# Kernel tuning notes

Measured on AMD Instinct MI355X. Metric: run time of the kernel, lower is better.

## Reference

```python
import jax, jax.numpy as jnp
import numpy as np


def setup_inputs() -> dict:
    key = jax.random.key(0)
    k1, k2, k3 = jax.random.split(key, 3)
    B, S, IN, OUT = 4, 2048, 4096, 4096
    # int8 activations, weights, bias (stored as int8; math accumulates in int32)
    x = jax.random.randint(k1, (B, S, IN), -127, 128, dtype=jnp.int32).astype(jnp.int8)
    weight = jax.random.randint(k2, (OUT, IN), -127, 128, dtype=jnp.int32).astype(jnp.int8)  # (out, in)
    bias = jax.random.randint(k3, (1, OUT), -127, 128, dtype=jnp.int32).astype(jnp.int8)
    alpha = jnp.float32(0.001)  # input_scale*weight_scale/output_scale
    beta = jnp.float32(0.01)    # bias_scale/output_scale
    return {"x": x, "weight": weight, "bias": bias, "alpha": alpha, "beta": beta}


def reference(x, weight, bias, alpha, beta):
    # Flatten leading dims: (B,S,IN) -> (N,IN)
    x_shape = x.shape
    xf = x.reshape(-1, x_shape[-1])
    acc = jax.lax.dot_general(
        xf, weight,
        dimension_numbers=(((1,), (1,)), ((), ())),
        preferred_element_type=jnp.int32,
    )  # (N, OUT) int32
    # Fused epilogue: y = round(alpha*acc + beta*bias), saturate to int8
    yf = alpha * acc.astype(jnp.float32) + beta * bias.astype(jnp.float32)
    y = jnp.clip(jnp.round(yf), -128.0, 127.0).astype(jnp.int8)
    return y.reshape(*x_shape[:-1], -1)
```

## Files before the change

kernel.cpp:

```cpp
#include <hip/hip_runtime.h>
#include <stdint.h>

using i32x4  = __attribute__((ext_vector_type(4)))  int;
using i32x16 = __attribute__((ext_vector_type(16))) int;

#define M_TOT 8192
#define N_TOT 4096
#define K_TOT 4096
#define BM 256
#define BN 256
#define BK 128
#define NT (K_TOT / BK)

__device__ __forceinline__ void gload_lds16(const void* g, void* l) {
  __builtin_amdgcn_global_load_lds(
      (const __attribute__((address_space(1))) void*)(uintptr_t)g,
      (__attribute__((address_space(3))) void*)(uint32_t)(uintptr_t)l,
      16, 0, 0);
}

__global__ void pack_tiles(const int* __restrict__ in, int8_t* __restrict__ out, int ngroups) {
  int stride = gridDim.x * blockDim.x;
  for (int idx = blockIdx.x * blockDim.x + threadIdx.x; idx < ngroups; idx += stride) {
    int sp = idx & 3;
    int rr = (idx >> 2) & 255;
    int kc = (idx >> 10) & 63;
    int p  = idx >> 16;
    int sl = sp ^ ((rr >> 1) & 3);
    const i32x4* src = (const i32x4*)(in + (((size_t)(p * 256 + rr)) << 12) + kc * 64 + sl * 16);
    i32x4 a = src[0], b = src[1], c = src[2], d = src[3];
    i32x4 o;
    o.x = (a.x & 255) | ((a.y & 255) << 8) | ((a.z & 255) << 16) | (a.w << 24);
    o.y = (b.x & 255) | ((b.y & 255) << 8) | ((b.z & 255) << 16) | (b.w << 24);
    o.z = (c.x & 255) | ((c.y & 255) << 8) | ((c.z & 255) << 16) | (c.w << 24);
    o.w = (d.x & 255) | ((d.y & 255) << 8) | ((d.z & 255) << 16) | (d.w << 24);
    ((i32x4*)out)[idx] = o;
  }
}

#define STAGE(srcbase, kc, ldsbuf, isB, h)                                          \
  { const int8_t* _g = (srcbase) + (size_t)(kc) * 16384 + w * 2048 + l * 16;        \
    char* _d = &lds[ldsbuf][(isB) * 32768 + (h) * 16384 + w * 2048];                \
    gload_lds16(_g, _d);                                                            \
    gload_lds16(_g + 1024, _d + 1024); }

__global__ __launch_bounds__(512, 2) void gemm_w8a8(
    const int8_t* __restrict__ Apack,
    const int8_t* __restrict__ Bpack,
    const int*    __restrict__ bias,
    const float*  __restrict__ alphap,
    const float*  __restrict__ betap,
    int* __restrict__ out)
{
  __shared__ __align__(16) char lds[2][65536];

  const int bid = blockIdx.x;
  const int wg  = (bid & 7) * 64 + (bid >> 3);
  const int tm  = wg & 31;
  const int tn  = wg >> 5;

  const int tid = threadIdx.x;
  const int w   = tid >> 6;
  const int l   = tid & 63;
  const int lr  = l & 31;
  const int hi  = l >> 5;
  const int wr  = w >> 2;
  const int wc  = w & 3;

  const int8_t* Asrc = Apack + (size_t)tm * (64 * 16384);
  const int8_t* Bsrc = Bpack + (size_t)tn * (64 * 16384);

  const int swz = (lr >> 1) & 3;
  int aRow[4], bRow[2], kOff[4];
#pragma unroll
  for (int mi = 0; mi < 4; ++mi) aRow[mi] = (wr * 128 + mi * 32 + lr) * 64;
#pragma unroll
  for (int ni = 0; ni < 2; ++ni) bRow[ni] = 32768 + (wc * 64 + ni * 32 + lr) * 64;
#pragma unroll
  for (int ks = 0; ks < 4; ++ks)
    kOff[ks] = (ks >> 1) * 16384 + (((((ks & 1) << 1) | hi)) ^ swz) * 16;

  i32x16 acc[4][2] = {};

  STAGE(Asrc, 0, 0, 0, 0);
  STAGE(Bsrc, 0, 0, 1, 0);
  STAGE(Asrc, 1, 0, 0, 1);
  STAGE(Bsrc, 1, 0, 1, 1);

  for (int t = 0; t < NT; ++t) {
    const int b  = t & 1;
    const int nb = b ^ 1;
    const char* L = lds[b];
    const bool more = (t + 1 < NT);
    const int kcn = 2 * (t + 1);
#pragma unroll
    for (int ks = 0; ks < 4; ++ks) {
      if ((ks & 1) == 0) {
        if (!more && ks == 2) { asm volatile("s_waitcnt vmcnt(0)" ::: "memory"); }
        else                  { asm volatile("s_waitcnt vmcnt(4)" ::: "memory"); }
        __builtin_amdgcn_s_barrier();
        __builtin_amdgcn_sched_barrier(0);
      }
      i32x4 af[4], bf[2];
      const int ko = kOff[ks];
#pragma unroll
      for (int mi = 0; mi < 4; ++mi) af[mi] = *(const i32x4*)(L + aRow[mi] + ko);
#pragma unroll
      for (int ni = 0; ni < 2; ++ni) bf[ni] = *(const i32x4*)(L + bRow[ni] + ko);
      if (more) {
        if (ks == 0) STAGE(Asrc, kcn,     nb, 0, 0);
        if (ks == 1) STAGE(Bsrc, kcn,     nb, 1, 0);
        if (ks == 2) STAGE(Asrc, kcn + 1, nb, 0, 1);
        if (ks == 3) STAGE(Bsrc, kcn + 1, nb, 1, 1);
      }
      asm volatile("s_waitcnt lgkmcnt(0)" ::: "memory");
      __builtin_amdgcn_sched_barrier(0);
      __builtin_amdgcn_s_setprio(1);
#pragma unroll
      for (int mi = 0; mi < 4; ++mi)
#pragma unroll
        for (int ni = 0; ni < 2; ++ni)
          acc[mi][ni] = __builtin_amdgcn_mfma_i32_32x32x32_i8(af[mi], bf[ni], acc[mi][ni], 0, 0, 0);
      __builtin_amdgcn_s_setprio(0);
    }
  }

  const float alpha = *alphap;
  const float beta  = *betap;
  const int brow = tm * BM, bcol = tn * BN;
#pragma unroll
  for (int ni = 0; ni < 2; ++ni) {
    const int col = bcol + wc * 64 + ni * 32 + lr;
    const float bb = beta * (float)bias[col];
#pragma unroll
    for (int mi = 0; mi < 4; ++mi) {
      const int rbase = brow + wr * 128 + mi * 32 + 4 * hi;
#pragma unroll
      for (int r = 0; r < 16; ++r) {
        const int row = rbase + (r & 3) + 8 * (r >> 2);
        float v = alpha * (float)acc[mi][ni][r] + bb;
        v = rintf(v);
        v = fminf(127.f, fmaxf(-128.f, v));
        out[(size_t)row * N_TOT + col] = (int)v;
      }
    }
  }
}

extern "C" void kernel_launch(void* const* d_in, const int* in_sizes, int n_in,
                              void* d_out, int out_size, void* d_ws, size_t ws_size,
                              hipStream_t stream) {
  const int*   x32    = (const int*)d_in[0];
  const int*   w32    = (const int*)d_in[1];
  const int*   bias   = (const int*)d_in[2];
  const float* alphap = (const float*)d_in[3];
  const float* betap  = (const float*)d_in[4];
  int* out = (int*)d_out;

  int8_t* xp = (int8_t*)d_ws;
  int8_t* wp = xp + (size_t)M_TOT * K_TOT;

  pack_tiles<<<2048, 256, 0, stream>>>(x32, xp, (M_TOT * K_TOT) / 16);
  pack_tiles<<<1024, 256, 0, stream>>>(w32, wp, (N_TOT * K_TOT) / 16);

  gemm_w8a8<<<512, 512, 0, stream>>>(xp, wp, bias, alphap, betap, out);
}
```

Baseline: 207.8 us.

## Use four-slot LDS ring with register double-buffered fragments and grouped tile mapping

Replaces the two-buffer LDS scheme with a four-slot ring of 64-wide K chunks, prefetching three chunks ahead. LDS fragment reads for the next sub-step are interleaved with the MFMAs of the current one through a/b register double buffering. It also remaps blocks to XCDs in 8x8 tile groups to improve L2 reuse, and merges the two pack kernels into one launch. The deeper pipeline uses more registers and makes the vmcnt accounting more complex.

```diff
diff --git a/kernel.cpp b/kernel.cpp
--- a/kernel.cpp
+++ b/kernel.cpp
@@ -9,8 +9,6 @@
 #define K_TOT 4096
 #define BM 256
 #define BN 256
-#define BK 128
-#define NT (K_TOT / BK)
 
 __device__ __forceinline__ void gload_lds16(const void* g, void* l) {
   __builtin_amdgcn_global_load_lds(
@@ -19,30 +17,72 @@
       16, 0, 0);
 }
 
-__global__ void pack_tiles(const int* __restrict__ in, int8_t* __restrict__ out, int ngroups) {
+__global__ void pack_tiles(const int* __restrict__ a32, const int* __restrict__ b32,
+                           int8_t* __restrict__ ap, int8_t* __restrict__ bp,
+                           int na, int ntot) {
   int stride = gridDim.x * blockDim.x;
-  for (int idx = blockIdx.x * blockDim.x + threadIdx.x; idx < ngroups; idx += stride) {
-    int sp = idx & 3;
-    int rr = (idx >> 2) & 255;
-    int kc = (idx >> 10) & 63;
-    int p  = idx >> 16;
+  for (int idx = blockIdx.x * blockDim.x + threadIdx.x; idx < ntot; idx += stride) {
+    int i = idx;
+    const int* src;
+    int8_t* dst;
+    if (idx < na) { src = a32; dst = ap; }
+    else          { src = b32; dst = bp; i = idx - na; }
+    int sp = i & 3;
+    int rr = (i >> 2) & 255;
+    int kc = (i >> 10) & 63;
+    int p  = i >> 16;
     int sl = sp ^ ((rr >> 1) & 3);
-    const i32x4* src = (const i32x4*)(in + (((size_t)(p * 256 + rr)) << 12) + kc * 64 + sl * 16);
-    i32x4 a = src[0], b = src[1], c = src[2], d = src[3];
+    const i32x4* s = (const i32x4*)(src + (((size_t)(p * 256 + rr)) << 12) + kc * 64 + sl * 16);
+    i32x4 a = s[0], b = s[1], c = s[2], d = s[3];
     i32x4 o;
     o.x = (a.x & 255) | ((a.y & 255) << 8) | ((a.z & 255) << 16) | (a.w << 24);
     o.y = (b.x & 255) | ((b.y & 255) << 8) | ((b.z & 255) << 16) | (b.w << 24);
     o.z = (c.x & 255) | ((c.y & 255) << 8) | ((c.z & 255) << 16) | (c.w << 24);
     o.w = (d.x & 255) | ((d.y & 255) << 8) | ((d.z & 255) << 16) | (d.w << 24);
-    ((i32x4*)out)[idx] = o;
+    ((i32x4*)dst)[i] = o;
   }
 }
 
-#define STAGE(srcbase, kc, ldsbuf, isB, h)                                          \
-  { const int8_t* _g = (srcbase) + (size_t)(kc) * 16384 + w * 2048 + l * 16;        \
-    char* _d = &lds[ldsbuf][(isB) * 32768 + (h) * 16384 + w * 2048];                \
-    gload_lds16(_g, _d);                                                            \
-    gload_lds16(_g + 1024, _d + 1024); }
+#define STAGE_H(jj, R) {                                                   \
+    const int8_t* _ga = Asrc + ((size_t)(jj) << 14) + stoff;               \
+    char* _da = lds + (((R) & 3) << 14) + w * 2048;                        \
+    gload_lds16(_ga, _da); gload_lds16(_ga + 1024, _da + 1024);            \
+    const int8_t* _gb = Bsrc + ((size_t)(jj) << 14) + stoff;               \
+    char* _db = lds + 65536 + (((R) & 3) << 14) + w * 2048;                \
+    gload_lds16(_gb, _db); gload_lds16(_gb + 1024, _db + 1024); }
+
+#define LOAD_FRAGS(DA, DB, R, S) {                                         \
+    const int _so = ((((S) << 1) | hi) ^ swz) * 16;                        \
+    const char* _pa = lds + (((R) & 3) << 14) + _so;                       \
+    const char* _pb = _pa + 65536;                                         \
+    _Pragma("unroll")                                                      \
+    for (int mi = 0; mi < 4; ++mi) DA[mi] = *(const i32x4*)(_pa + aRow[mi]); \
+    _Pragma("unroll")                                                      \
+    for (int ni = 0; ni < 2; ++ni) DB[ni] = *(const i32x4*)(_pb + bRow[ni]); }
+
+#define MFMA8(A, B)                                                        \
+    _Pragma("unroll")                                                      \
+    for (int mi = 0; mi < 4; ++mi)                                         \
+    _Pragma("unroll")                                                      \
+    for (int ni = 0; ni < 2; ++ni)                                         \
+      acc[mi][ni] = __builtin_amdgcn_mfma_i32_32x32x32_i8(A[mi], B[ni], acc[mi][ni], 0, 0, 0);
+
+#define INTERVAL(j, R0, R1, VM, DO_STAGE, DO_NEXT) {                       \
+    asm volatile("s_waitcnt vmcnt(" VM ")" ::: "memory");                  \
+    __builtin_amdgcn_s_barrier();                                          \
+    __builtin_amdgcn_sched_barrier(0);                                     \
+    if (DO_STAGE) STAGE_H((j) + 3, (R0) + 3);                              \
+    LOAD_FRAGS(a1, b1, R0, 1)                                              \
+    __builtin_amdgcn_sched_barrier(0);                                     \
+    __builtin_amdgcn_s_setprio(1);                                         \
+    MFMA8(a0, b0)                                                          \
+    __builtin_amdgcn_s_setprio(0);                                         \
+    __builtin_amdgcn_sched_barrier(0);                                     \
+    if (DO_NEXT) LOAD_FRAGS(a0, b0, R1, 0)                                 \
+    __builtin_amdgcn_sched_barrier(0);                                     \
+    __builtin_amdgcn_s_setprio(1);                                         \
+    MFMA8(a1, b1)                                                          \
+    __builtin_amdgcn_s_setprio(0); }
 
 __global__ __launch_bounds__(512, 2) void gemm_w8a8(
     const int8_t* __restrict__ Apack,
@@ -52,12 +92,12 @@
     const float*  __restrict__ betap,
     int* __restrict__ out)
 {
-  __shared__ __align__(16) char lds[2][65536];
+  __shared__ __align__(16) char lds[131072];
 
   const int bid = blockIdx.x;
-  const int wg  = (bid & 7) * 64 + (bid >> 3);
-  const int tm  = wg & 31;
-  const int tn  = wg >> 5;
+  const int xcd = bid & 7, wi = bid >> 3;
+  const int tm = (xcd & 3) * 8 + (wi & 7);
+  const int tn = (xcd >> 2) * 8 + (wi >> 3);
 
   const int tid = threadIdx.x;
   const int w   = tid >> 6;
@@ -66,64 +106,40 @@
   const int hi  = l >> 5;
   const int wr  = w >> 2;
   const int wc  = w & 3;
+  const int stoff = w * 2048 + l * 16;
 
   const int8_t* Asrc = Apack + (size_t)tm * (64 * 16384);
   const int8_t* Bsrc = Bpack + (size_t)tn * (64 * 16384);
 
   const int swz = (lr >> 1) & 3;
-  int aRow[4], bRow[2], kOff[4];
+  int aRow[4], bRow[2];
 #pragma unroll
   for (int mi = 0; mi < 4; ++mi) aRow[mi] = (wr * 128 + mi * 32 + lr) * 64;
 #pragma unroll
-  for (int ni = 0; ni < 2; ++ni) bRow[ni] = 32768 + (wc * 64 + ni * 32 + lr) * 64;
-#pragma unroll
-  for (int ks = 0; ks < 4; ++ks)
-    kOff[ks] = (ks >> 1) * 16384 + (((((ks & 1) << 1) | hi)) ^ swz) * 16;
+  for (int ni = 0; ni < 2; ++ni) bRow[ni] = (wc * 64 + ni * 32 + lr) * 64;
 
   i32x16 acc[4][2] = {};
+  i32x4 a0[4], b0[2], a1[4], b1[2];
 
-  STAGE(Asrc, 0, 0, 0, 0);
-  STAGE(Bsrc, 0, 0, 1, 0);
-  STAGE(Asrc, 1, 0, 0, 1);
-  STAGE(Bsrc, 1, 0, 1, 1);
+  STAGE_H(0, 0)
+  STAGE_H(1, 1)
+  STAGE_H(2, 2)
+  asm volatile("s_waitcnt vmcnt(8)" ::: "memory");
+  __builtin_amdgcn_s_barrier();
+  __builtin_amdgcn_sched_barrier(0);
+  LOAD_FRAGS(a0, b0, 0, 0)
 
-  for (int t = 0; t < NT; ++t) {
-    const int b  = t & 1;
-    const int nb = b ^ 1;
-    const char* L = lds[b];
-    const bool more = (t + 1 < NT);
-    const int kcn = 2 * (t + 1);
-#pragma unroll
-    for (int ks = 0; ks < 4; ++ks) {
-      if ((ks & 1) == 0) {
-        if (!more && ks == 2) { asm volatile("s_waitcnt vmcnt(0)" ::: "memory"); }
-        else                  { asm volatile("s_waitcnt vmcnt(4)" ::: "memory"); }
-        __builtin_amdgcn_s_barrier();
-        __builtin_amdgcn_sched_barrier(0);
-      }
-      i32x4 af[4], bf[2];
-      const int ko = kOff[ks];
-#pragma unroll
-      for (int mi = 0; mi < 4; ++mi) af[mi] = *(const i32x4*)(L + aRow[mi] + ko);
-#pragma unroll
-      for (int ni = 0; ni < 2; ++ni) bf[ni] = *(const i32x4*)(L + bRow[ni] + ko);
-      if (more) {
-        if (ks == 0) STAGE(Asrc, kcn,     nb, 0, 0);
-        if (ks == 1) STAGE(Bsrc, kcn,     nb, 1, 0);
-        if (ks == 2) STAGE(Asrc, kcn + 1, nb, 0, 1);
-        if (ks == 3) STAGE(Bsrc, kcn + 1, nb, 1, 1);
-      }
-      asm volatile("s_waitcnt lgkmcnt(0)" ::: "memory");
-      __builtin_amdgcn_sched_barrier(0);
-      __builtin_amdgcn_s_setprio(1);
-#pragma unroll
-      for (int mi = 0; mi < 4; ++mi)
-#pragma unroll
-        for (int ni = 0; ni < 2; ++ni)
-          acc[mi][ni] = __builtin_amdgcn_mfma_i32_32x32x32_i8(af[mi], bf[ni], acc[mi][ni], 0, 0, 0);
-      __builtin_amdgcn_s_setprio(0);
-    }
+  for (int tt = 0; tt < 15; ++tt) {
+    const int j0 = tt * 4;
+    INTERVAL(j0 + 0, 0, 1, "4", 1, 1)
+    INTERVAL(j0 + 1, 1, 2, "4", 1, 1)
+    INTERVAL(j0 + 2, 2, 3, "4", 1, 1)
+    INTERVAL(j0 + 3, 3, 0, "4", 1, 1)
   }
+  INTERVAL(60, 0, 1, "4", 1, 1)
+  INTERVAL(61, 1, 2, "4", 0, 1)
+  INTERVAL(62, 2, 3, "0", 0, 1)
+  INTERVAL(63, 3, 0, "0", 0, 0)
 
   const float alpha = *alphap;
   const float beta  = *betap;
@@ -160,8 +176,9 @@
   int8_t* xp = (int8_t*)d_ws;
   int8_t* wp = xp + (size_t)M_TOT * K_TOT;
 
-  pack_tiles<<<2048, 256, 0, stream>>>(x32, xp, (M_TOT * K_TOT) / 16);
-  pack_tiles<<<1024, 256, 0, stream>>>(w32, wp, (N_TOT * K_TOT) / 16);
+  const int na   = (M_TOT * K_TOT) / 16;
+  const int ntot = na + (N_TOT * K_TOT) / 16;
+  pack_tiles<<<3072, 256, 0, stream>>>(x32, w32, xp, wp, na, ntot);
 
   gemm_w8a8<<<512, 512, 0, stream>>>(xp, wp, bias, alphap, betap, out);
 }
```

Measured after the change: 200.6 us. 1.04x faster.
